# Performance work log

Hardware: AMD Instinct MI355X
Metric: run time of the kernel (lower is better)

The kernel has to match this reference:

```python
import jax, jax.numpy as jnp
import numpy as np

B, N, D = 2, 4096, 512
H, P = 8, 9            # num_heads, n_points
HD = D // H            # head_dim
OFFSET_SCALE = 4.0


def setup_inputs() -> dict:
    key = jax.random.key(0)
    ks = jax.random.split(key, 8)
    g = lambda k, shape, s: jax.random.normal(k, shape, jnp.float32) * s
    return {
        "x": jax.random.normal(ks[0], (B, N, D), jnp.float32),
        "Wq": g(ks[1], (D, D), 0.02),
        "bq": jnp.zeros((D,), jnp.float32),
        # offset predictor (original inits to zero; randomized small for a nontrivial test)
        "Woff": g(ks[2], (H * P * 2, D), 0.05),
        "boff": g(ks[3], (H * P * 2,), 0.05),
        # 1x1 conv producing k/v maps == a D -> 2D linear on tokens
        "Wkv": g(ks[4], (2 * D, D), 0.02),
        "bkv": jnp.zeros((2 * D,), jnp.float32),
        "Wo": g(ks[5], (D, D), 0.02),
        "bo": jnp.zeros((D,), jnp.float32),
        "h": 16,
        "w": 256,
    }


def _bilinear_zeros(feat, sx, sy, h, w):
    """grid_sample(mode=bilinear, padding=zeros, align_corners=True).
    feat: (B, H, N, hd) with N = h*w row-major; sx, sy: (B, H, S) pixel coords.
    Returns (B, H, S, hd). (align_corners=True normalize/denormalize round-trip
    in the original is the identity, so we sample at pixel coords directly.)
    """
    x0 = jnp.floor(sx)
    y0 = jnp.floor(sy)
    wx1 = sx - x0
    wy1 = sy - y0

    def corner(xi, yi, wgt):
        valid = ((xi >= 0) & (xi < w) & (yi >= 0) & (yi < h)).astype(feat.dtype)
        idx = (jnp.clip(yi, 0, h - 1) * w + jnp.clip(xi, 0, w - 1)).astype(jnp.int32)
        val = jnp.take_along_axis(feat, idx[..., None], axis=2)  # (B,H,S,hd)
        return val * (wgt * valid)[..., None]

    return (corner(x0, y0, (1 - wx1) * (1 - wy1))
            + corner(x0 + 1, y0, wx1 * (1 - wy1))
            + corner(x0, y0 + 1, (1 - wx1) * wy1)
            + corner(x0 + 1, y0 + 1, wx1 * wy1))


def reference(x, Wq, bq, Woff, boff, Wkv, bkv, Wo, bo, h, w):
    b, n, d = x.shape
    # queries, split heads -> (B,H,N,hd)
    q = (x @ Wq.T + bq).reshape(b, n, H, HD).transpose(0, 2, 1, 3)
    # per-query, per-head offsets in pixels: (B,N,H,P,2) (dx,dy)
    off = jnp.tanh(x @ Woff.T + boff).reshape(b, n, H, P, 2) * OFFSET_SCALE
    # 1x1 conv -> k/v token maps, split heads -> (B,H,N,hd)
    kv = x @ Wkv.T + bkv
    k = kv[..., :d].reshape(b, n, H, HD).transpose(0, 2, 1, 3)
    v = kv[..., d:].reshape(b, n, H, HD).transpose(0, 2, 1, 3)
    # base pixel grid (x,y) per token
    tok = jnp.arange(n)
    base = jnp.stack([(tok % w).astype(x.dtype), (tok // w).astype(x.dtype)], -1)  # (N,2)
    samp = base[None, :, None, None, :] + off          # (B,N,H,P,2)
    samp = samp.transpose(0, 2, 1, 3, 4).reshape(b, H, n * P, 2)
    sk = _bilinear_zeros(k, samp[..., 0], samp[..., 1], h, w).reshape(b, H, n, P, HD)
    sv = _bilinear_zeros(v, samp[..., 0], samp[..., 1], h, w).reshape(b, H, n, P, HD)
    logits = jnp.einsum('bhnd,bhnpd->bhnp', q, sk) * (HD ** -0.5)
    attn = jax.nn.softmax(logits, axis=-1)
    out = jnp.einsum('bhnp,bhnpd->bhnd', attn, sv)
    out = out.transpose(0, 2, 1, 3).reshape(b, n, d)   # merge heads
    return out @ Wo.T + bo
```

## Files before the change

### kernel.cpp

```cpp
#include <hip/hip_runtime.h>
#include <hip/hip_bf16.h>

static constexpr int B_  = 2;
static constexpr int N_  = 4096;
static constexpr int D_  = 512;
static constexpr int H_  = 8;
static constexpr int P_  = 9;
static constexpr int GH_ = 16;
static constexpr int GW_ = 256;
static constexpr int M_  = B_ * N_;

typedef __attribute__((ext_vector_type(8))) short bf16x8;
typedef __attribute__((ext_vector_type(4))) float f32x4;

__device__ __forceinline__ unsigned short f2b(float f) {
    __hip_bfloat16 h = __float2bfloat16(f);
    return *reinterpret_cast<unsigned short*>(&h);
}
__device__ __forceinline__ float b2f(unsigned short u) {
    return __uint_as_float(((unsigned int)u) << 16);
}
__device__ __forceinline__ float b2f_lo(unsigned int u) { return __uint_as_float(u << 16); }
__device__ __forceinline__ float b2f_hi(unsigned int u) { return __uint_as_float(u & 0xffff0000u); }

__global__ __launch_bounds__(256) void cast_multi(
    const float* __restrict__ x,   const float* __restrict__ wq,
    const float* __restrict__ wkv, const float* __restrict__ wo,
    const float* __restrict__ woff,
    unsigned short* __restrict__ x_hi, unsigned short* __restrict__ x_lo,
    unsigned short* __restrict__ wall, unsigned short* __restrict__ wob) {
    int g = blockIdx.x * 256 + threadIdx.x;

    if (g < 1048576) {
        float4 v = reinterpret_cast<const float4*>(x)[g];
        ushort4 hi, lo;
        hi.x = f2b(v.x); hi.y = f2b(v.y); hi.z = f2b(v.z); hi.w = f2b(v.w);
        lo.x = f2b(v.x - b2f(hi.x)); lo.y = f2b(v.y - b2f(hi.y));
        lo.z = f2b(v.z - b2f(hi.z)); lo.w = f2b(v.w - b2f(hi.w));
        reinterpret_cast<ushort4*>(x_hi)[g] = hi;
        reinterpret_cast<ushort4*>(x_lo)[g] = lo;
        return;
    }
    g -= 1048576;
    if (g < 65536) {
        float4 v = reinterpret_cast<const float4*>(wq)[g];
        ushort4 o; o.x = f2b(v.x); o.y = f2b(v.y); o.z = f2b(v.z); o.w = f2b(v.w);
        reinterpret_cast<ushort4*>(wall)[g] = o;
        return;
    }
    g -= 65536;
    if (g < 131072) {
        float4 v = reinterpret_cast<const float4*>(wkv)[g];
        ushort4 o; o.x = f2b(v.x); o.y = f2b(v.y); o.z = f2b(v.z); o.w = f2b(v.w);
        reinterpret_cast<ushort4*>(wall)[65536 + g] = o;
        return;
    }
    g -= 131072;
    if (g < 65536) {
        float4 v = reinterpret_cast<const float4*>(wo)[g];
        ushort4 o; o.x = f2b(v.x); o.y = f2b(v.y); o.z = f2b(v.z); o.w = f2b(v.w);
        reinterpret_cast<ushort4*>(wob)[g] = o;
        return;
    }
    g -= 65536;
    if (g < 18432) {
        float4 v = reinterpret_cast<const float4*>(woff)[g];
        ushort4 hi, lo;
        hi.x = f2b(v.x); hi.y = f2b(v.y); hi.z = f2b(v.z); hi.w = f2b(v.w);
        lo.x = f2b(v.x - b2f(hi.x)); lo.y = f2b(v.y - b2f(hi.y));
        lo.z = f2b(v.z - b2f(hi.z)); lo.w = f2b(v.w - b2f(hi.w));
        reinterpret_cast<ushort4*>(wall)[196608 + g] = hi;
        reinterpret_cast<ushort4*>(wall)[229376 + g] = lo;
        reinterpret_cast<ushort4*>(wall)[262144 + g] = hi;
        return;
    }
    g -= 18432;
    const int which = g / 14336;
    const int idx   = g - which * 14336;
    ushort4 z = {0, 0, 0, 0};
    reinterpret_cast<ushort4*>(wall)[215040 + which * 32768 + idx] = z;
}

__device__ __forceinline__ void gemm_seg(const unsigned short* __restrict__ A,
                                         const unsigned short* __restrict__ W,
                                         int m0, int n0, int Kloop, int lda, int ldw,
                                         short* As, short* Bs,
                                         f32x4 (&acc)[4][2], int wave, int lane) {
    const int gi = wave * 64 + lane;
    const int r0 = gi >> 2, c0 = (gi & 3) * 8;

    const unsigned short* pa0 = A + (size_t)(m0 + r0) * lda + c0;
    const unsigned short* pa1 = A + (size_t)(m0 + 64 + r0) * lda + c0;
    const unsigned short* pw  = W + (size_t)(n0 + r0) * ldw + c0;

    const int wm = wave & 1, wn = wave >> 1;
    const int fr = lane & 15;
    const int fk = (lane >> 4) * 8;

    for (int k0 = 0; k0 < Kloop; k0 += 64) {
#pragma unroll
        for (int t = 0; t < 2; ++t) {
            __builtin_amdgcn_global_load_lds(
                (const __attribute__((address_space(1))) void*)(pa0 + k0 + t * 32),
                (__attribute__((address_space(3))) void*)(As + t * 4096 + wave * 512),
                16, 0, 0);
            __builtin_amdgcn_global_load_lds(
                (const __attribute__((address_space(1))) void*)(pa1 + k0 + t * 32),
                (__attribute__((address_space(3))) void*)(As + t * 4096 + 2048 + wave * 512),
                16, 0, 0);
            __builtin_amdgcn_global_load_lds(
                (const __attribute__((address_space(1))) void*)(pw + k0 + t * 32),
                (__attribute__((address_space(3))) void*)(Bs + t * 2048 + wave * 512),
                16, 0, 0);
        }
        __syncthreads();

#pragma unroll
        for (int t = 0; t < 2; ++t) {
            bf16x8 af[4], bf[2];
#pragma unroll
            for (int i = 0; i < 4; ++i)
                af[i] = *reinterpret_cast<const bf16x8*>(
                    &As[t * 4096 + (wm * 64 + i * 16 + fr) * 32 + fk]);
#pragma unroll
            for (int j = 0; j < 2; ++j)
                bf[j] = *reinterpret_cast<const bf16x8*>(
                    &Bs[t * 2048 + (wn * 32 + j * 16 + fr) * 32 + fk]);
#pragma unroll
            for (int i = 0; i < 4; ++i)
#pragma unroll
                for (int j = 0; j < 2; ++j)
                    acc[i][j] = __builtin_amdgcn_mfma_f32_16x16x32_bf16(
                        af[i], bf[j], acc[i][j], 0, 0, 0);
        }
        __syncthreads();
    }
}

__global__ __launch_bounds__(256, 3) void gemm_fused(
    const unsigned short* __restrict__ x_hi,
    const unsigned short* __restrict__ x_lo,
    const unsigned short* __restrict__ wall,
    const float* __restrict__ bq,
    const float* __restrict__ bkv,
    const float* __restrict__ boff,
    unsigned short* __restrict__ q_bf,
    unsigned short* __restrict__ k_bf,
    unsigned short* __restrict__ v_bf,
    float* __restrict__ off1,
    float* __restrict__ off2,
    float* __restrict__ off3) {
    __shared__ short As[8192];
    __shared__ short Bs[4096];
    const int t = threadIdx.x;
    const int wave = t >> 6, lane = t & 63;
    const int m0 = blockIdx.y * 128;
    const int n0 = blockIdx.x * 64;

    const unsigned short* A = (blockIdx.x >= 32) ? x_lo : x_hi;

    f32x4 acc[4][2] = {};
    gemm_seg(A, wall, m0, n0, 512, 512, 512, As, Bs, acc, wave, lane);

    const int wm = wave & 1, wn = wave >> 1;
    const int ecol = lane & 15;
    const int erow = (lane >> 4) * 4;
#pragma unroll
    for (int i = 0; i < 4; ++i) {
#pragma unroll
        for (int j = 0; j < 2; ++j) {
            const int n = n0 + wn * 32 + j * 16 + ecol;
#pragma unroll
            for (int r = 0; r < 4; ++r) {
                const int m = m0 + wm * 64 + i * 16 + erow + r;
                const float v = acc[i][j][r];
                if (n < 512) {
                    q_bf[(size_t)m * 512 + n] = f2b((v + bq[n]) * 0.125f);
                } else if (n < 1024) {
                    k_bf[(size_t)m * 512 + (n - 512)] = f2b(v + bkv[n - 512]);
                } else if (n < 1536) {
                    v_bf[(size_t)m * 512 + (n - 1024)] = f2b(v + bkv[n - 512]);
                } else if (n < 1792) {
                    const int c = n - 1536;
                    if (c < 144) off1[(size_t)m * 144 + c] = v + boff[c];
                } else if (n < 2048) {
                    const int c = n - 1792;
                    if (c < 144) off2[(size_t)m * 144 + c] = v;
                } else {
                    const int c = n - 2048;
                    if (c < 144) off3[(size_t)m * 144 + c] = v;
                }
            }
        }
    }
}

__global__ __launch_bounds__(256, 3) void gemm_out(
    const unsigned short* __restrict__ A,
    const unsigned short* __restrict__ W,
    const float* __restrict__ bias,
    float* __restrict__ out) {
    __shared__ short As[8192];
    __shared__ short Bs[4096];
    const int t = threadIdx.x;
    const int wave = t >> 6, lane = t & 63;
    const int m0 = blockIdx.y * 128;
    const int n0 = blockIdx.x * 64;

    f32x4 acc[4][2] = {};
    gemm_seg(A, W, m0, n0, 512, 512, 512, As, Bs, acc, wave, lane);

    const int wm = wave & 1, wn = wave >> 1;
    const int ecol = lane & 15;
    const int erow = (lane >> 4) * 4;
#pragma unroll
    for (int i = 0; i < 4; ++i) {
#pragma unroll
        for (int j = 0; j < 2; ++j) {
            const int n = n0 + wn * 32 + j * 16 + ecol;
            const float bb = bias[n];
#pragma unroll
            for (int r = 0; r < 4; ++r) {
                const int m = m0 + wm * 64 + i * 16 + erow + r;
                out[(size_t)m * 512 + n] = acc[i][j][r] + bb;
            }
        }
    }
}

__global__ __launch_bounds__(256) void attn_sample(const unsigned short* __restrict__ q_bf,
                                                   const float* __restrict__ off1,
                                                   const float* __restrict__ off2,
                                                   const float* __restrict__ off3,
                                                   const unsigned short* __restrict__ k_bf,
                                                   const unsigned short* __restrict__ v_bf,
                                                   unsigned short* __restrict__ a_bf) {
    __shared__ float4 pw_s[4][36];
    __shared__ int4   po_s[4][36];

    const int lane = threadIdx.x & 63;
    const int wave = threadIdx.x >> 6;
    const int quarter = lane >> 4;
    const int j    = lane & 15;
    const int wid  = blockIdx.x * 4 + wave;
    const int b    = wid >> 13;
    const int hh   = (wid >> 10) & 7;
    const int nq   = wid & 1023;
    const int n    = nq * 4 + quarter;

    if (lane < 36) {
        const int qt = lane / 9;
        const int p  = lane - qt * 9;
        const int tn = nq * 4 + qt;
        const size_t tokq = (size_t)b * N_ + tn;
        const size_t oidx = tokq * 144 + hh * 18 + 2 * p;
        const float2 a1 = *reinterpret_cast<const float2*>(off1 + oidx);
        const float2 a2 = *reinterpret_cast<const float2*>(off2 + oidx);
        const float2 a3 = *reinterpret_cast<const float2*>(off3 + oidx);
        const float dx = tanhf(a1.x + a2.x + a3.x) * 4.0f;
        const float dy = tanhf(a1.y + a2.y + a3.y) * 4.0f;
        const float sx = (float)(tn & (GW_ - 1)) + dx;
        const float sy = (float)(tn >> 8) + dy;
        const float x0f = floorf(sx), y0f = floorf(sy);
        const int x0 = (int)x0f, y0 = (int)y0f;
        const float wx1 = sx - x0f, wy1 = sy - y0f;
        const float wx0 = 1.0f - wx1, wy0 = 1.0f - wy1;

        float4 w;
        int4 ro;
        {
            const int xi = x0, yi = y0;
            const bool v = (xi >= 0) & (xi < GW_) & (yi >= 0) & (yi < GH_);
            w.x = v ? wx0 * wy0 : 0.0f;
            const int xc = xi < 0 ? 0 : (xi > 255 ? 255 : xi);
            const int yc = yi < 0 ? 0 : (yi > 15 ? 15 : yi);
            ro.x = (yc * GW_ + xc) * 512 + hh * 64;
        }
        {
            const int xi = x0 + 1, yi = y0;
            const bool v = (xi >= 0) & (xi < GW_) & (yi >= 0) & (yi < GH_);
            w.y = v ? wx1 * wy0 : 0.0f;
            const int xc = xi < 0 ? 0 : (xi > 255 ? 255 : xi);
            const int yc = yi < 0 ? 0 : (yi > 15 ? 15 : yi);
            ro.y = (yc * GW_ + xc) * 512 + hh * 64;
        }
        {
            const int xi = x0, yi = y0 + 1;
            const bool v = (xi >= 0) & (xi < GW_) & (yi >= 0) & (yi < GH_);
            w.z = v ? wx0 * wy1 : 0.0f;
            const int xc = xi < 0 ? 0 : (xi > 255 ? 255 : xi);
            const int yc = yi < 0 ? 0 : (yi > 15 ? 15 : yi);
            ro.z = (yc * GW_ + xc) * 512 + hh * 64;
        }
        {
            const int xi = x0 + 1, yi = y0 + 1;
            const bool v = (xi >= 0) & (xi < GW_) & (yi >= 0) & (yi < GH_);
            w.w = v ? wx1 * wy1 : 0.0f;
            const int xc = xi < 0 ? 0 : (xi > 255 ? 255 : xi);
            const int yc = yi < 0 ? 0 : (yi > 15 ? 15 : yi);
            ro.w = (yc * GW_ + xc) * 512 + hh * 64;
        }
        pw_s[wave][lane] = w;
        po_s[wave][lane] = ro;
    }
    __syncthreads();

    const size_t tok = (size_t)b * N_ + n;
    const uint2 qp = *reinterpret_cast<const uint2*>(
        q_bf + tok * 512 + hh * 64 + 4 * j);
    const float q0 = b2f_lo(qp.x), q1 = b2f_hi(qp.x);
    const float q2 = b2f_lo(qp.y), q3 = b2f_hi(qp.y);

    const unsigned short* kbase = k_bf + (size_t)b * (N_ * 512) + 4 * j;
    const unsigned short* vbase = v_bf + (size_t)b * (N_ * 512) + 4 * j;
    const int ebase = quarter * 9;

    float lg[9], s0[9], s1[9], s2[9], s3[9];
    float mx = -1e30f;

#pragma unroll
    for (int p = 0; p < P_; ++p) {
        const float4 w = pw_s[wave][ebase + p];
        const int4 ro = po_s[wave][ebase + p];
        float k0 = 0.f, k1 = 0.f, k2 = 0.f, k3 = 0.f;
        float v0 = 0.f, v1 = 0.f, v2 = 0.f, v3 = 0.f;
#pragma unroll
        for (int c = 0; c < 4; ++c) {
            const int r = (c == 0) ? ro.x : (c == 1) ? ro.y : (c == 2) ? ro.z : ro.w;
            const float wgt = (c == 0) ? w.x : (c == 1) ? w.y : (c == 2) ? w.z : w.w;
            const uint2 ku = *reinterpret_cast<const uint2*>(kbase + r);
            const uint2 vu = *reinterpret_cast<const uint2*>(vbase + r);
            k0 = fmaf(wgt, b2f_lo(ku.x), k0); k1 = fmaf(wgt, b2f_hi(ku.x), k1);
            k2 = fmaf(wgt, b2f_lo(ku.y), k2); k3 = fmaf(wgt, b2f_hi(ku.y), k3);
            v0 = fmaf(wgt, b2f_lo(vu.x), v0); v1 = fmaf(wgt, b2f_hi(vu.x), v1);
            v2 = fmaf(wgt, b2f_lo(vu.y), v2); v3 = fmaf(wgt, b2f_hi(vu.y), v3);
        }
        float ts = fmaf(q0, k0, fmaf(q1, k1, fmaf(q2, k2, q3 * k3)));
#pragma unroll
        for (int s = 8; s > 0; s >>= 1) ts += __shfl_xor(ts, s, 64);
        lg[p] = ts;
        s0[p] = v0; s1[p] = v1; s2[p] = v2; s3[p] = v3;
        mx = fmaxf(mx, lg[p]);
    }

    float ssum = 0.f, o0 = 0.f, o1 = 0.f, o2 = 0.f, o3 = 0.f;
#pragma unroll
    for (int p = 0; p < P_; ++p) {
        const float e = __expf(lg[p] - mx);
        ssum += e;
        o0 = fmaf(e, s0[p], o0);
        o1 = fmaf(e, s1[p], o1);
        o2 = fmaf(e, s2[p], o2);
        o3 = fmaf(e, s3[p], o3);
    }
    const float rs = 1.0f / ssum;
    uint2 pack;
    pack.x = (unsigned int)f2b(o0 * rs) | ((unsigned int)f2b(o1 * rs) << 16);
    pack.y = (unsigned int)f2b(o2 * rs) | ((unsigned int)f2b(o3 * rs) << 16);
    *reinterpret_cast<uint2*>(a_bf + tok * 512 + hh * 64 + 4 * j) = pack;
}

extern "C" void kernel_launch(void* const* d_in, const int* in_sizes, int n_in,
                              void* d_out, int out_size, void* d_ws, size_t ws_size,
                              hipStream_t stream) {
    const float* x    = (const float*)d_in[0];
    const float* bq   = (const float*)d_in[2];
    const float* Woff = (const float*)d_in[3];
    const float* boff = (const float*)d_in[4];
    const float* bkv  = (const float*)d_in[6];
    const float* bo   = (const float*)d_in[8];
    float* out = (float*)d_out;

    char* ws = (char*)d_ws;
    unsigned short* q_bf    = (unsigned short*)ws; ws += (size_t)M_ * 512 * 2;
    unsigned short* k_bf    = (unsigned short*)ws; ws += (size_t)M_ * 512 * 2;
    unsigned short* v_bf    = (unsigned short*)ws; ws += (size_t)M_ * 512 * 2;
    float*          off1    = (float*)ws;          ws += (size_t)M_ * 144 * 4;
    float*          off2    = (float*)ws;          ws += (size_t)M_ * 144 * 4;
    float*          off3    = (float*)ws;          ws += (size_t)M_ * 144 * 4;
    unsigned short* xlo_abf = (unsigned short*)ws; ws += (size_t)M_ * 512 * 2;
    unsigned short* x_hi    = (unsigned short*)ws; ws += (size_t)M_ * 512 * 2;
    unsigned short* wall    = (unsigned short*)ws; ws += (size_t)2304 * 512 * 2;
    unsigned short* wob     = (unsigned short*)ws; ws += (size_t)512 * 512 * 2;

    const dim3 blk(256);

    cast_multi<<<dim3(5360), blk, 0, stream>>>(
        x, (const float*)d_in[1], (const float*)d_in[5], (const float*)d_in[7], Woff,
        x_hi, xlo_abf, wall, wob);

    gemm_fused<<<dim3(36, M_ / 128), blk, 0, stream>>>(
        x_hi, xlo_abf, wall, bq, bkv, boff, q_bf, k_bf, v_bf, off1, off2, off3);

    attn_sample<<<dim3((B_ * H_ * N_) / 16), blk, 0, stream>>>(
        q_bf, off1, off2, off3, k_bf, v_bf, xlo_abf);

    gemm_out<<<dim3(8, M_ / 128), blk, 0, stream>>>(xlo_abf, wob, bo, out);
}
```

Baseline: 180.5 us.

## Double-buffer LDS tiles in GEMM kernels to overlap loads with MFMA

Replaces the single-buffered GEMM main loop with a ping-pong scheme using two LDS buffers for A and B tiles. The next K-slab is prefetched via global_load_lds while the MFMAs for the current slab run, which is meant to hide global memory latency behind compute. LDS use per block doubles to 48 KB, which may limit occupancy under the launch bound of 3 blocks per CU. Correctness relies on the synchronisation placement between staging and compute.

```diff
diff --git a/kernel.cpp b/kernel.cpp
--- a/kernel.cpp
+++ b/kernel.cpp
@@ -81,11 +81,57 @@
     reinterpret_cast<ushort4*>(wall)[215040 + which * 32768 + idx] = z;
 }
 
-__device__ __forceinline__ void gemm_seg(const unsigned short* __restrict__ A,
-                                         const unsigned short* __restrict__ W,
-                                         int m0, int n0, int Kloop, int lda, int ldw,
-                                         short* As, short* Bs,
-                                         f32x4 (&acc)[4][2], int wave, int lane) {
+
+__device__ __forceinline__ void stage_tiles(const unsigned short* pa0,
+                                            const unsigned short* pa1,
+                                            const unsigned short* pw,
+                                            int k0, short* Ab, short* Bb, int wave) {
+#pragma unroll
+    for (int t = 0; t < 2; ++t) {
+        __builtin_amdgcn_global_load_lds(
+            (const __attribute__((address_space(1))) void*)(pa0 + k0 + t * 32),
+            (__attribute__((address_space(3))) void*)(Ab + t * 4096 + wave * 512),
+            16, 0, 0);
+        __builtin_amdgcn_global_load_lds(
+            (const __attribute__((address_space(1))) void*)(pa1 + k0 + t * 32),
+            (__attribute__((address_space(3))) void*)(Ab + t * 4096 + 2048 + wave * 512),
+            16, 0, 0);
+        __builtin_amdgcn_global_load_lds(
+            (const __attribute__((address_space(1))) void*)(pw + k0 + t * 32),
+            (__attribute__((address_space(3))) void*)(Bb + t * 2048 + wave * 512),
+            16, 0, 0);
+    }
+}
+
+__device__ __forceinline__ void compute_tiles(const short* Ab, const short* Bb,
+                                              f32x4 (&acc)[4][2],
+                                              int wm, int wn, int fr, int fk) {
+#pragma unroll
+    for (int t = 0; t < 2; ++t) {
+        bf16x8 af[4], bf[2];
+#pragma unroll
+        for (int i = 0; i < 4; ++i)
+            af[i] = *reinterpret_cast<const bf16x8*>(
+                &Ab[t * 4096 + (wm * 64 + i * 16 + fr) * 32 + fk]);
+#pragma unroll
+        for (int j = 0; j < 2; ++j)
+            bf[j] = *reinterpret_cast<const bf16x8*>(
+                &Bb[t * 2048 + (wn * 32 + j * 16 + fr) * 32 + fk]);
+#pragma unroll
+        for (int i = 0; i < 4; ++i)
+#pragma unroll
+            for (int j = 0; j < 2; ++j)
+                acc[i][j] = __builtin_amdgcn_mfma_f32_16x16x32_bf16(
+                    af[i], bf[j], acc[i][j], 0, 0, 0);
+    }
+}
+
+__device__ __forceinline__ void gemm_seg_db(const unsigned short* __restrict__ A,
+                                            const unsigned short* __restrict__ W,
+                                            int m0, int n0, int Kloop, int lda, int ldw,
+                                            short* As0, short* As1,
+                                            short* Bs0, short* Bs1,
+                                            f32x4 (&acc)[4][2], int wave, int lane) {
     const int gi = wave * 64 + lane;
     const int r0 = gi >> 2, c0 = (gi & 3) * 8;
 
@@ -97,43 +143,19 @@
     const int fr = lane & 15;
     const int fk = (lane >> 4) * 8;
 
-    for (int k0 = 0; k0 < Kloop; k0 += 64) {
-#pragma unroll
-        for (int t = 0; t < 2; ++t) {
-            __builtin_amdgcn_global_load_lds(
-                (const __attribute__((address_space(1))) void*)(pa0 + k0 + t * 32),
-                (__attribute__((address_space(3))) void*)(As + t * 4096 + wave * 512),
-                16, 0, 0);
-            __builtin_amdgcn_global_load_lds(
-                (const __attribute__((address_space(1))) void*)(pa1 + k0 + t * 32),
-                (__attribute__((address_space(3))) void*)(As + t * 4096 + 2048 + wave * 512),
-                16, 0, 0);
-            __builtin_amdgcn_global_load_lds(
-                (const __attribute__((address_space(1))) void*)(pw + k0 + t * 32),
-                (__attribute__((address_space(3))) void*)(Bs + t * 2048 + wave * 512),
-                16, 0, 0);
-        }
+    stage_tiles(pa0, pa1, pw, 0, As0, Bs0, wave);
+
+    for (int k0 = 0; k0 < Kloop; k0 += 128) {
         __syncthreads();
-
-#pragma unroll
-        for (int t = 0; t < 2; ++t) {
-            bf16x8 af[4], bf[2];
-#pragma unroll
-            for (int i = 0; i < 4; ++i)
-                af[i] = *reinterpret_cast<const bf16x8*>(
-                    &As[t * 4096 + (wm * 64 + i * 16 + fr) * 32 + fk]);
-#pragma unroll
-            for (int j = 0; j < 2; ++j)
-                bf[j] = *reinterpret_cast<const bf16x8*>(
-                    &Bs[t * 2048 + (wn * 32 + j * 16 + fr) * 32 + fk]);
-#pragma unroll
-            for (int i = 0; i < 4; ++i)
-#pragma unroll
-                for (int j = 0; j < 2; ++j)
-                    acc[i][j] = __builtin_amdgcn_mfma_f32_16x16x32_bf16(
-                        af[i], bf[j], acc[i][j], 0, 0, 0);
-        }
+        if (k0 + 64 < Kloop)
+            stage_tiles(pa0, pa1, pw, k0 + 64, As1, Bs1, wave);
+        compute_tiles(As0, Bs0, acc, wm, wn, fr, fk);
+
         __syncthreads();
+        if (k0 + 128 < Kloop)
+            stage_tiles(pa0, pa1, pw, k0 + 128, As0, Bs0, wave);
+        if (k0 + 64 < Kloop)
+            compute_tiles(As1, Bs1, acc, wm, wn, fr, fk);
     }
 }
 
@@ -150,8 +172,8 @@
     float* __restrict__ off1,
     float* __restrict__ off2,
     float* __restrict__ off3) {
-    __shared__ short As[8192];
-    __shared__ short Bs[4096];
+    __shared__ short As0[8192], As1[8192];
+    __shared__ short Bs0[4096], Bs1[4096];
     const int t = threadIdx.x;
     const int wave = t >> 6, lane = t & 63;
     const int m0 = blockIdx.y * 128;
@@ -160,7 +182,7 @@
     const unsigned short* A = (blockIdx.x >= 32) ? x_lo : x_hi;
 
     f32x4 acc[4][2] = {};
-    gemm_seg(A, wall, m0, n0, 512, 512, 512, As, Bs, acc, wave, lane);
+    gemm_seg_db(A, wall, m0, n0, 512, 512, 512, As0, As1, Bs0, Bs1, acc, wave, lane);
 
     const int wm = wave & 1, wn = wave >> 1;
     const int ecol = lane & 15;
@@ -200,15 +222,15 @@
     const unsigned short* __restrict__ W,
     const float* __restrict__ bias,
     float* __restrict__ out) {
-    __shared__ short As[8192];
-    __shared__ short Bs[4096];
+    __shared__ short As0[8192], As1[8192];
+    __shared__ short Bs0[4096], Bs1[4096];
     const int t = threadIdx.x;
     const int wave = t >> 6, lane = t & 63;
     const int m0 = blockIdx.y * 128;
     const int n0 = blockIdx.x * 64;
 
     f32x4 acc[4][2] = {};
-    gemm_seg(A, W, m0, n0, 512, 512, 512, As, Bs, acc, wave, lane);
+    gemm_seg_db(A, W, m0, n0, 512, 512, 512, As0, As1, Bs0, Bs1, acc, wave, lane);
 
     const int wm = wave & 1, wn = wave >> 1;
     const int ecol = lane & 15;
```

New measurement: 187.7 us. 4.0% more time.
